# Optimization experiments

Hardware: AMD Instinct MI355X
Metric: run time of the kernel (lower is better)

## Reference

```python
import jax, jax.numpy as jnp
import numpy as np

B, H, W, D = 8, 64, 64, 256   # batch, grid rows, grid cols, q_size==c_size
N = 1024                      # number of query/alignment points
R_WIN, C_WIN = 1, 2           # hardcoded window half-sizes from the module


def setup_inputs() -> dict:
    key = jax.random.key(0)
    k1, k2, k3, k4 = jax.random.split(key, 4)
    q = jax.random.normal(k1, (B, H, W, D), jnp.float32)
    c_t = jax.random.normal(k2, (B, N, D), jnp.float32)
    # float positions inside the grid: row in [0,H-1), col in [0,W-1)
    p_t = jax.random.uniform(k3, (B, N, 2), jnp.float32) * jnp.array([H - 1, W - 1], jnp.float32)
    W_a = jax.random.normal(k4, (D, D), jnp.float32) / np.sqrt(D)  # nn.Linear(q_size->c_size) weight [c,q]
    return {"q": q, "c_t": c_t, "p_t": p_t, "W_a": W_a}


def reference(q, c_t, p_t, W_a):
    Bq, Hh, Ww, Dd = q.shape
    rows, cols = Hh + 1, Ww + 1
    # ConstantPad2d((1,0,1,0), nan) on channels-first layout == pad top row & left col with NaN
    q_pad = jnp.pad(q.transpose(0, 3, 1, 2), ((0, 0), (0, 0), (1, 0), (1, 0)),
                    constant_values=jnp.nan)                      # [B,D,rows,cols]
    p0 = p_t[..., 0].astype(jnp.int32)
    p1 = p_t[..., 1].astype(jnp.int32)
    r = jnp.clip(p0[..., None] + jnp.arange(-R_WIN, R_WIN + 1) + 1, 0, rows) % rows  # [B,N,2R+1]
    c = jnp.clip(p1[..., None] + jnp.arange(-C_WIN, C_WIN + 1) + 1, 0, cols) % cols  # [B,N,2C+1]
    # flattened window indices, i (row offset) major, j (col offset) minor
    idx = (r[..., :, None] * cols + c[..., None, :]).reshape(Bq, r.shape[1], -1)     # [B,N,K]
    K = idx.shape[-1]
    q_flat = q_pad.reshape(Bq, Dd, rows * cols).transpose(0, 2, 1)                   # [B,rows*cols,D]
    qg = jnp.take_along_axis(q_flat, idx.reshape(Bq, -1, 1), axis=1)
    qg = qg.reshape(Bq, idx.shape[1], K, Dd)                                          # [B,N,K,D]
    nan_loc = jnp.isnan(qg[..., 0])                                                   # [B,N,K]
    qg = jnp.where(nan_loc[..., None], 0.0, qg)
    # Gaussian decay around the (float) predicted position
    rexp = jnp.exp(-2.0 * ((jnp.clip(r.astype(q.dtype) - 1, 0, None) - p_t[..., 0:1]) / R_WIN) ** 2)
    cexp = jnp.exp(-2.0 * ((jnp.clip(c.astype(q.dtype) - 1, 0, None) - p_t[..., 1:2]) / C_WIN) ** 2)
    expw = (rexp[..., :, None] * cexp[..., None, :]).reshape(Bq, r.shape[1], K)       # [B,N,K]
    # score: (W_a qg) . c_t per (b,n)
    Wa = jnp.einsum('bnkd,cd->bnkc', qg, W_a)
    a_t = jnp.einsum('bnkc,bnc->bnk', Wa, c_t)
    a_t = jnp.where(nan_loc, -jnp.inf, a_t)
    W_attn = jax.nn.softmax(a_t, axis=2) * expw
    return jnp.einsum('bnk,bnkd->bnd', W_attn, qg)                                    # [B,N,D]
```

## Files before the change

kernel.cpp:

```cpp
#include <hip/hip_runtime.h>
#include <math.h>

#define BATCH   8
#define HGRID   64
#define WGRID   64
#define DDIM    256
#define NPTS    1024
#define ROWS    65
#define COLS    65
#define KWIN    15
#define BN      (BATCH*NPTS)

#define PIDS_PER_BLK 16
#define THREADS      512
#define NREG         9
#define NLDS         6

typedef __attribute__((ext_vector_type(8))) short bf16x8;
typedef __attribute__((ext_vector_type(4))) float f32x4;

__device__ __forceinline__ void gload_lds16(const float* src, float* dst) {
    __builtin_amdgcn_global_load_lds(
        (const __attribute__((address_space(1))) unsigned int*)src,
        (__attribute__((address_space(3))) unsigned int*)dst, 16, 0, 0);
}

__global__ __launch_bounds__(THREADS, 4) void fused_local_attn(
        const float* __restrict__ q,
        const float* __restrict__ c_t,
        const float* __restrict__ p_t,
        const float* __restrict__ W,
        float* __restrict__ out) {

    __shared__ __align__(16) float smem[NLDS * DDIM * 8];
    float (*Pr)[DDIM] = reinterpret_cast<float (*)[DDIM]>(smem);

    const int t    = threadIdx.x;
    const int w    = t >> 6;
    const int lane = t & 63;
    const int l15  = lane & 15;
    const int g    = lane >> 4;
    const int bid  = blockIdx.x;
    const int wk   = (bid & 7) * 64 + (bid >> 3);
    const int pid0 = wk * PIDS_PER_BLK;
    const int dq   = w * 32;
    float* qsw = smem + w * (NLDS * DDIM);

    f32x4 acc0 = (f32x4)0.f;
    f32x4 acc1 = (f32x4)0.f;

    const float* ap  = &c_t[(size_t)(pid0 + l15) * DDIM + g * 8];
    const float* wp0 = &W[(size_t)(g * 8) * DDIM + dq + l15];
    const float* wp1 = wp0 + 16;

    #pragma unroll 2
    for (int kt = 0; kt < 8; ++kt) {
        const float4 a01 = *reinterpret_cast<const float4*>(ap + kt * 32);
        const float4 a23 = *reinterpret_cast<const float4*>(ap + kt * 32 + 4);
        const float af[8] = {a01.x, a01.y, a01.z, a01.w, a23.x, a23.y, a23.z, a23.w};
        union { bf16x8 v; unsigned u[4]; } AH, AL;
        #pragma unroll
        for (int i = 0; i < 4; ++i) {
            const unsigned u0 = __float_as_uint(af[2 * i]);
            const unsigned u1 = __float_as_uint(af[2 * i + 1]);
            AH.u[i] = __builtin_amdgcn_perm(u1, u0, 0x07060302u);
            const float l0 = af[2 * i]     - __uint_as_float(u0 & 0xFFFF0000u);
            const float l1 = af[2 * i + 1] - __uint_as_float(u1 & 0xFFFF0000u);
            AL.u[i] = __builtin_amdgcn_perm(__float_as_uint(l1), __float_as_uint(l0),
                                            0x07060302u);
        }

        #pragma unroll
        for (int df = 0; df < 2; ++df) {
            const float* wp = (df == 0) ? wp0 : wp1;
            float bf[8];
            #pragma unroll
            for (int i = 0; i < 8; ++i)
                bf[i] = wp[(size_t)(kt * 32 + i) * DDIM];
            union { bf16x8 v; unsigned u[4]; } BH, BL;
            #pragma unroll
            for (int i = 0; i < 4; ++i) {
                const unsigned u0 = __float_as_uint(bf[2 * i]);
                const unsigned u1 = __float_as_uint(bf[2 * i + 1]);
                BH.u[i] = __builtin_amdgcn_perm(u1, u0, 0x07060302u);
                const float l0 = bf[2 * i]     - __uint_as_float(u0 & 0xFFFF0000u);
                const float l1 = bf[2 * i + 1] - __uint_as_float(u1 & 0xFFFF0000u);
                BL.u[i] = __builtin_amdgcn_perm(__float_as_uint(l1), __float_as_uint(l0),
                                                0x07060302u);
            }
            f32x4 a = (df == 0) ? acc0 : acc1;
            a = __builtin_amdgcn_mfma_f32_16x16x32_bf16(AH.v, BH.v, a, 0, 0, 0);
            a = __builtin_amdgcn_mfma_f32_16x16x32_bf16(AH.v, BL.v, a, 0, 0, 0);
            a = __builtin_amdgcn_mfma_f32_16x16x32_bf16(AL.v, BH.v, a, 0, 0, 0);
            if (df == 0) acc0 = a; else acc1 = a;
        }
    }

    #pragma unroll
    for (int r = 0; r < 4; ++r) {
        Pr[g * 4 + r][dq +  0 + l15] = acc0[r];
        Pr[g * 4 + r][dq + 16 + l15] = acc1[r];
    }
    __syncthreads();

    const float4 prA = *reinterpret_cast<const float4*>(&Pr[w * 2 + 0][lane * 4]);
    const float4 prB = *reinterpret_cast<const float4*>(&Pr[w * 2 + 1][lane * 4]);
    __syncthreads();

    #pragma unroll 1
    for (int pp = 0; pp < 2; ++pp) {
        const int pl  = w * 2 + pp;
        const int pid = pid0 + pl;
        const int b   = pid >> 10;
        const float4 pr = pp ? prB : prA;
        const float2 ppos = *reinterpret_cast<const float2*>(&p_t[pid * 2]);
        const float p0f = ppos.x;
        const float p1f = ppos.y;
        const int p0 = (int)p0f;
        const int p1 = (int)p1f;

        float re[3], ce[5];
        int rowidx[3], colidx[5];
        #pragma unroll
        for (int i = 0; i < 3; ++i) {
            int rr = p0 + i;
            rr = rr > ROWS ? ROWS : rr;
            rr = (rr == ROWS) ? 0 : rr;
            rowidx[i] = rr;
            const float rf = (float)(rr - 1 > 0 ? rr - 1 : 0);
            const float dr = rf - p0f;
            re[i] = __expf(-2.0f * dr * dr);
        }
        #pragma unroll
        for (int j = 0; j < 5; ++j) {
            int cc = p1 + j - 1;
            cc = cc < 0 ? 0 : (cc > COLS ? COLS : cc);
            cc = (cc == COLS) ? 0 : cc;
            colidx[j] = cc;
            const float cf = (float)(cc - 1 > 0 ? cc - 1 : 0);
            const float dc = (cf - p1f) * 0.5f;
            ce[j] = __expf(-2.0f * dc * dc);
        }

        asm volatile("s_waitcnt lgkmcnt(0)" ::: "memory");
        __builtin_amdgcn_sched_barrier(0);

        float4 qg[NREG];
        unsigned vmask = 0;
        #pragma unroll
        for (int k = 0; k < KWIN; ++k) {
            const int i = k / 5, j = k % 5;
            const int rr = rowidx[i];
            const int cc = colidx[j];
            const bool valid = (rr != 0) && (cc != 0);
            const float* src =
                &q[((size_t)((b * HGRID + rr - 1) * WGRID + cc - 1)) * DDIM + lane * 4];
            if (k < NREG) {
                float4 v = make_float4(0.f, 0.f, 0.f, 0.f);
                if (valid) v = *reinterpret_cast<const float4*>(src);
                qg[k] = v;
            } else {
                if (valid) gload_lds16(src, &qsw[(k - NREG) * DDIM]);
            }
            if (valid) vmask |= (1u << k);
        }
        asm volatile("s_waitcnt vmcnt(0)" ::: "memory");
        #pragma unroll
        for (int k = 0; k < NREG; ++k)
            asm volatile("" : "+v"(qg[k].x), "+v"(qg[k].y), "+v"(qg[k].z), "+v"(qg[k].w));

        float score[KWIN];
        #pragma unroll
        for (int k = 0; k < NREG; ++k) {
            const float4 v = qg[k];
            score[k] = fmaf(v.x, pr.x, fmaf(v.y, pr.y, fmaf(v.z, pr.z, v.w * pr.w)));
        }
        #pragma unroll
        for (int k = NREG; k < KWIN; ++k) {
            const float4 v =
                *reinterpret_cast<const float4*>(&qsw[(k - NREG) * DDIM + lane * 4]);
            score[k] = fmaf(v.x, pr.x, fmaf(v.y, pr.y, fmaf(v.z, pr.z, v.w * pr.w)));
        }

        #pragma unroll
        for (int k = 0; k < KWIN; ++k) {
            float s = score[k];
            #pragma unroll
            for (int off = 32; off; off >>= 1) s += __shfl_xor(s, off, 64);
            score[k] = ((vmask >> k) & 1u) ? s : -INFINITY;
        }

        float mx = score[0];
        #pragma unroll
        for (int k = 1; k < KWIN; ++k) mx = fmaxf(mx, score[k]);
        float sum = 0.f;
        #pragma unroll
        for (int k = 0; k < KWIN; ++k) {
            const float e = __expf(score[k] - mx);
            score[k] = e;
            sum += e;
        }
        const float inv = 1.0f / sum;

        float ox = 0.f, oy = 0.f, oz = 0.f, ow = 0.f;
        #pragma unroll
        for (int k = 0; k < KWIN; ++k) {
            const int i = k / 5, j = k % 5;
            const float wk2 = score[k] * inv * re[i] * ce[j];
            if (k < NREG) {
                ox = fmaf(wk2, qg[k].x, ox);
                oy = fmaf(wk2, qg[k].y, oy);
                oz = fmaf(wk2, qg[k].z, oz);
                ow = fmaf(wk2, qg[k].w, ow);
            } else if ((vmask >> k) & 1u) {
                const float4 v =
                    *reinterpret_cast<const float4*>(&qsw[(k - NREG) * DDIM + lane * 4]);
                ox = fmaf(wk2, v.x, ox);
                oy = fmaf(wk2, v.y, oy);
                oz = fmaf(wk2, v.z, oz);
                ow = fmaf(wk2, v.w, ow);
            }
        }
        *reinterpret_cast<float4*>(&out[(size_t)pid * DDIM + lane * 4]) =
            make_float4(ox, oy, oz, ow);
    }
}

extern "C" void kernel_launch(void* const* d_in, const int* in_sizes, int n_in,
                              void* d_out, int out_size, void* d_ws, size_t ws_size,
                              hipStream_t stream) {
    const float* q   = (const float*)d_in[0];
    const float* c_t = (const float*)d_in[1];
    const float* p_t = (const float*)d_in[2];
    const float* W_a = (const float*)d_in[3];
    float* out = (float*)d_out;

    fused_local_attn<<<BN / PIDS_PER_BLK, THREADS, 0, stream>>>(q, c_t, p_t, W_a, out);
}
```

Before: 33.72 us.

## Software-pipeline the two points per wave by prefetching the second point's window

Unrolls the per-wave loop over its two query points into a two-stage pipeline. The second point's register-resident window loads are issued before the first point's score and softmax computation, using a partial vmcnt wait. The second point's LDS-bound loads and Gaussian weights are issued and computed while its register loads are still in flight. This aims to hide global-memory latency, at the cost of more live registers (two sets of float4 windows), which may lower occupancy. The hardcoded vmcnt(9) assumes all nine second-point register loads were issued, which does not hold at grid edges.

```diff
diff --git a/kernel.cpp b/kernel.cpp
--- a/kernel.cpp
+++ b/kernel.cpp
@@ -107,89 +107,124 @@
     const float4 prB = *reinterpret_cast<const float4*>(&Pr[w * 2 + 1][lane * 4]);
     __syncthreads();
 
-    #pragma unroll 1
-    for (int pp = 0; pp < 2; ++pp) {
-        const int pl  = w * 2 + pp;
-        const int pid = pid0 + pl;
-        const int b   = pid >> 10;
-        const float4 pr = pp ? prB : prA;
-        const float2 ppos = *reinterpret_cast<const float2*>(&p_t[pid * 2]);
-        const float p0f = ppos.x;
-        const float p1f = ppos.y;
-        const int p0 = (int)p0f;
-        const int p1 = (int)p1f;
-
-        float re[3], ce[5];
-        int rowidx[3], colidx[5];
+    const int pidA = pid0 + w * 2 + 0;
+    const int pidB = pid0 + w * 2 + 1;
+    const int bb   = pidA >> 10;
+
+    const float2 posA = *reinterpret_cast<const float2*>(&p_t[pidA * 2]);
+    const float2 posB = *reinterpret_cast<const float2*>(&p_t[pidB * 2]);
+
+    float reA[3], ceA[5];
+    int rowA[3], colA[5];
+    {
+        const int p0 = (int)posA.x, p1 = (int)posA.y;
         #pragma unroll
         for (int i = 0; i < 3; ++i) {
             int rr = p0 + i;
             rr = rr > ROWS ? ROWS : rr;
             rr = (rr == ROWS) ? 0 : rr;
-            rowidx[i] = rr;
+            rowA[i] = rr;
             const float rf = (float)(rr - 1 > 0 ? rr - 1 : 0);
-            const float dr = rf - p0f;
-            re[i] = __expf(-2.0f * dr * dr);
+            const float dr = rf - posA.x;
+            reA[i] = __expf(-2.0f * dr * dr);
         }
         #pragma unroll
         for (int j = 0; j < 5; ++j) {
             int cc = p1 + j - 1;
             cc = cc < 0 ? 0 : (cc > COLS ? COLS : cc);
             cc = (cc == COLS) ? 0 : cc;
-            colidx[j] = cc;
+            colA[j] = cc;
             const float cf = (float)(cc - 1 > 0 ? cc - 1 : 0);
-            const float dc = (cf - p1f) * 0.5f;
-            ce[j] = __expf(-2.0f * dc * dc);
-        }
-
-        asm volatile("s_waitcnt lgkmcnt(0)" ::: "memory");
-        __builtin_amdgcn_sched_barrier(0);
-
-        float4 qg[NREG];
-        unsigned vmask = 0;
-        #pragma unroll
-        for (int k = 0; k < KWIN; ++k) {
-            const int i = k / 5, j = k % 5;
-            const int rr = rowidx[i];
-            const int cc = colidx[j];
-            const bool valid = (rr != 0) && (cc != 0);
-            const float* src =
-                &q[((size_t)((b * HGRID + rr - 1) * WGRID + cc - 1)) * DDIM + lane * 4];
-            if (k < NREG) {
-                float4 v = make_float4(0.f, 0.f, 0.f, 0.f);
-                if (valid) v = *reinterpret_cast<const float4*>(src);
-                qg[k] = v;
-            } else {
-                if (valid) gload_lds16(src, &qsw[(k - NREG) * DDIM]);
-            }
-            if (valid) vmask |= (1u << k);
-        }
-        asm volatile("s_waitcnt vmcnt(0)" ::: "memory");
-        #pragma unroll
-        for (int k = 0; k < NREG; ++k)
-            asm volatile("" : "+v"(qg[k].x), "+v"(qg[k].y), "+v"(qg[k].z), "+v"(qg[k].w));
-
+            const float dc = (cf - posA.y) * 0.5f;
+            ceA[j] = __expf(-2.0f * dc * dc);
+        }
+    }
+    int rowB[3], colB[5];
+    {
+        const int p0 = (int)posB.x, p1 = (int)posB.y;
+        #pragma unroll
+        for (int i = 0; i < 3; ++i) {
+            int rr = p0 + i;
+            rr = rr > ROWS ? ROWS : rr;
+            rr = (rr == ROWS) ? 0 : rr;
+            rowB[i] = rr;
+        }
+        #pragma unroll
+        for (int j = 0; j < 5; ++j) {
+            int cc = p1 + j - 1;
+            cc = cc < 0 ? 0 : (cc > COLS ? COLS : cc);
+            cc = (cc == COLS) ? 0 : cc;
+            colB[j] = cc;
+        }
+    }
+
+    float4 qgA[NREG];
+    unsigned vmA = 0;
+    #pragma unroll
+    for (int k = 0; k < KWIN; ++k) {
+        const int i = k / 5, j = k % 5;
+        const int rr = rowA[i], cc = colA[j];
+        const bool valid = (rr != 0) && (cc != 0);
+        const float* src =
+            &q[((size_t)((bb * HGRID + rr - 1) * WGRID + cc - 1)) * DDIM + lane * 4];
+        if (k < NREG) {
+            float4 v = make_float4(0.f, 0.f, 0.f, 0.f);
+            if (valid) v = *reinterpret_cast<const float4*>(src);
+            qgA[k] = v;
+        } else {
+            if (valid) gload_lds16(src, &qsw[(k - NREG) * DDIM]);
+        }
+        if (valid) vmA |= (1u << k);
+    }
+
+    __builtin_amdgcn_sched_barrier(0);
+
+    float4 qgB[NREG];
+    unsigned vmB = 0;
+    #pragma unroll
+    for (int k = 0; k < NREG; ++k) {
+        const int i = k / 5, j = k % 5;
+        const int rr = rowB[i], cc = colB[j];
+        const bool valid = (rr != 0) && (cc != 0);
+        float4 v = make_float4(0.f, 0.f, 0.f, 0.f);
+        if (valid) {
+            v = *reinterpret_cast<const float4*>(
+                &q[((size_t)((bb * HGRID + rr - 1) * WGRID + cc - 1)) * DDIM + lane * 4]);
+            vmB |= (1u << k);
+        }
+        qgB[k] = v;
+    }
+    #pragma unroll
+    for (int k = NREG; k < KWIN; ++k) {
+        const int i = k / 5, j = k % 5;
+        if ((rowB[i] != 0) && (colB[j] != 0)) vmB |= (1u << k);
+    }
+
+    asm volatile("s_waitcnt vmcnt(9)" ::: "memory");
+    #pragma unroll
+    for (int k = 0; k < NREG; ++k)
+        asm volatile("" : "+v"(qgA[k].x), "+v"(qgA[k].y), "+v"(qgA[k].z), "+v"(qgA[k].w));
+
+    {
         float score[KWIN];
         #pragma unroll
         for (int k = 0; k < NREG; ++k) {
-            const float4 v = qg[k];
-            score[k] = fmaf(v.x, pr.x, fmaf(v.y, pr.y, fmaf(v.z, pr.z, v.w * pr.w)));
+            const float4 v = qgA[k];
+            score[k] = fmaf(v.x, prA.x, fmaf(v.y, prA.y, fmaf(v.z, prA.z, v.w * prA.w)));
         }
         #pragma unroll
         for (int k = NREG; k < KWIN; ++k) {
             const float4 v =
                 *reinterpret_cast<const float4*>(&qsw[(k - NREG) * DDIM + lane * 4]);
-            score[k] = fmaf(v.x, pr.x, fmaf(v.y, pr.y, fmaf(v.z, pr.z, v.w * pr.w)));
-        }
-
+            score[k] = fmaf(v.x, prA.x, fmaf(v.y, prA.y, fmaf(v.z, prA.z, v.w * prA.w)));
+        }
         #pragma unroll
         for (int k = 0; k < KWIN; ++k) {
             float s = score[k];
             #pragma unroll
             for (int off = 32; off; off >>= 1) s += __shfl_xor(s, off, 64);
-            score[k] = ((vmask >> k) & 1u) ? s : -INFINITY;
-        }
-
+            score[k] = ((vmA >> k) & 1u) ? s : -INFINITY;
+        }
         float mx = score[0];
         #pragma unroll
         for (int k = 1; k < KWIN; ++k) mx = fmaxf(mx, score[k]);
@@ -206,13 +241,13 @@
         #pragma unroll
         for (int k = 0; k < KWIN; ++k) {
             const int i = k / 5, j = k % 5;
-            const float wk2 = score[k] * inv * re[i] * ce[j];
+            const float wk2 = score[k] * inv * reA[i] * ceA[j];
             if (k < NREG) {
-                ox = fmaf(wk2, qg[k].x, ox);
-                oy = fmaf(wk2, qg[k].y, oy);
-                oz = fmaf(wk2, qg[k].z, oz);
-                ow = fmaf(wk2, qg[k].w, ow);
-            } else if ((vmask >> k) & 1u) {
+                ox = fmaf(wk2, qgA[k].x, ox);
+                oy = fmaf(wk2, qgA[k].y, oy);
+                oz = fmaf(wk2, qgA[k].z, oz);
+                ow = fmaf(wk2, qgA[k].w, ow);
+            } else if ((vmA >> k) & 1u) {
                 const float4 v =
                     *reinterpret_cast<const float4*>(&qsw[(k - NREG) * DDIM + lane * 4]);
                 ox = fmaf(wk2, v.x, ox);
@@ -221,7 +256,98 @@
                 ow = fmaf(wk2, v.w, ow);
             }
         }
-        *reinterpret_cast<float4*>(&out[(size_t)pid * DDIM + lane * 4]) =
+        *reinterpret_cast<float4*>(&out[(size_t)pidA * DDIM + lane * 4]) =
+            make_float4(ox, oy, oz, ow);
+    }
+
+    asm volatile("s_waitcnt lgkmcnt(0)" ::: "memory");
+    __builtin_amdgcn_sched_barrier(0);
+    #pragma unroll
+    for (int k = NREG; k < KWIN; ++k) {
+        const int i = k / 5, j = k % 5;
+        const int rr = rowB[i], cc = colB[j];
+        if ((rr != 0) && (cc != 0)) {
+            gload_lds16(&q[((size_t)((bb * HGRID + rr - 1) * WGRID + cc - 1)) * DDIM
+                           + lane * 4],
+                        &qsw[(k - NREG) * DDIM]);
+        }
+    }
+
+    float reB[3], ceB[5];
+    {
+        #pragma unroll
+        for (int i = 0; i < 3; ++i) {
+            const int rr = rowB[i];
+            const float rf = (float)(rr - 1 > 0 ? rr - 1 : 0);
+            const float dr = rf - posB.x;
+            reB[i] = __expf(-2.0f * dr * dr);
+        }
+        #pragma unroll
+        for (int j = 0; j < 5; ++j) {
+            const int cc = colB[j];
+            const float cf = (float)(cc - 1 > 0 ? cc - 1 : 0);
+            const float dc = (cf - posB.y) * 0.5f;
+            ceB[j] = __expf(-2.0f * dc * dc);
+        }
+    }
+
+    asm volatile("s_waitcnt vmcnt(0)" ::: "memory");
+    #pragma unroll
+    for (int k = 0; k < NREG; ++k)
+        asm volatile("" : "+v"(qgB[k].x), "+v"(qgB[k].y), "+v"(qgB[k].z), "+v"(qgB[k].w));
+
+    {
+        float score[KWIN];
+        #pragma unroll
+        for (int k = 0; k < NREG; ++k) {
+            const float4 v = qgB[k];
+            score[k] = fmaf(v.x, prB.x, fmaf(v.y, prB.y, fmaf(v.z, prB.z, v.w * prB.w)));
+        }
+        #pragma unroll
+        for (int k = NREG; k < KWIN; ++k) {
+            const float4 v =
+                *reinterpret_cast<const float4*>(&qsw[(k - NREG) * DDIM + lane * 4]);
+            score[k] = fmaf(v.x, prB.x, fmaf(v.y, prB.y, fmaf(v.z, prB.z, v.w * prB.w)));
+        }
+        #pragma unroll
+        for (int k = 0; k < KWIN; ++k) {
+            float s = score[k];
+            #pragma unroll
+            for (int off = 32; off; off >>= 1) s += __shfl_xor(s, off, 64);
+            score[k] = ((vmB >> k) & 1u) ? s : -INFINITY;
+        }
+        float mx = score[0];
+        #pragma unroll
+        for (int k = 1; k < KWIN; ++k) mx = fmaxf(mx, score[k]);
+        float sum = 0.f;
+        #pragma unroll
+        for (int k = 0; k < KWIN; ++k) {
+            const float e = __expf(score[k] - mx);
+            score[k] = e;
+            sum += e;
+        }
+        const float inv = 1.0f / sum;
+
+        float ox = 0.f, oy = 0.f, oz = 0.f, ow = 0.f;
+        #pragma unroll
+        for (int k = 0; k < KWIN; ++k) {
+            const int i = k / 5, j = k % 5;
+            const float wk2 = score[k] * inv * reB[i] * ceB[j];
+            if (k < NREG) {
+                ox = fmaf(wk2, qgB[k].x, ox);
+                oy = fmaf(wk2, qgB[k].y, oy);
+                oz = fmaf(wk2, qgB[k].z, oz);
+                ow = fmaf(wk2, qgB[k].w, ow);
+            } else if ((vmB >> k) & 1u) {
+                const float4 v =
+                    *reinterpret_cast<const float4*>(&qsw[(k - NREG) * DDIM + lane * 4]);
+                ox = fmaf(wk2, v.x, ox);
+                oy = fmaf(wk2, v.y, oy);
+                oz = fmaf(wk2, v.z, oz);
+                ow = fmaf(wk2, v.w, ow);
+            }
+        }
+        *reinterpret_cast<float4*>(&out[(size_t)pidB * DDIM + lane * 4]) =
             make_float4(ox, oy, oz, ow);
     }
 }
```

Result: slower. 35.55 us (+5.4%).
